# Optimization experiments

Hardware: AMD Instinct MI355X
Metric: run time of the kernel (lower is better)

Reference implementation:

```python
import jax, jax.numpy as jnp
import numpy as np

PAD_IDX, BOS_IDX, EOS_IDX = 0, 1, 2
NUM_LABELS = 48
B, T = 1024, 512
NEG = -10000.0


def make_trans(key):
    trans = jax.random.normal(key, (NUM_LABELS, NUM_LABELS), dtype=jnp.float32)
    trans = trans.at[BOS_IDX, :].set(NEG)
    trans = trans.at[:, EOS_IDX].set(NEG)
    trans = trans.at[:, PAD_IDX].set(NEG)
    trans = trans.at[PAD_IDX, :].set(NEG)
    trans = trans.at[PAD_IDX, EOS_IDX].set(0.0)
    trans = trans.at[PAD_IDX, PAD_IDX].set(0.0)
    return trans


def setup_inputs() -> dict:
    key = jax.random.key(0)
    k_h, k_tr = jax.random.split(key)
    h = jax.random.normal(k_h, (B, T, NUM_LABELS), dtype=jnp.float32)
    mask = jnp.ones((B, T), dtype=jnp.float32)
    trans = make_trans(k_tr)
    return {"h": h, "mask": mask, "trans": trans, "batch_size": B}


def reference(h, mask, trans, batch_size):
    # h: (B, T, L), mask: (B, T), trans: (L, L)
    L = trans.shape[0]
    score0 = jnp.full((batch_size, L), NEG, dtype=h.dtype).at[:, BOS_IDX].set(0.0)

    def step(score, inp):
        h_t, m_t = inp            # h_t: (B, L), m_t: (B,)
        # new[b, i] = logsumexp_j(score[b, j] + h_t[b, i] + trans[i, j])
        z = score[:, None, :] + h_t[:, :, None] + trans[None, :, :]  # (B, L, L)
        score_t = jax.nn.logsumexp(z, axis=-1)
        m = m_t[:, None]
        score = score_t * m + score * (1.0 - m)
        return score, None

    # scan over time: move T to leading axis
    score, _ = jax.lax.scan(step, score0, (jnp.swapaxes(h, 0, 1), jnp.swapaxes(mask, 0, 1)))
    return jax.nn.logsumexp(score, axis=-1)  # (B,)
```

## Files before the change

kernel.cpp:

```cpp
#include <hip/hip_runtime.h>
#include <math.h>

namespace {
constexpr int L = 48;
constexpr int OCT = 8;
constexpr float LN2f = 0.69314718055994530942f;
}

__global__ __launch_bounds__(64, 1)
void crf_fwd(const float* __restrict__ h,
             const float* __restrict__ mask,
             const float* __restrict__ trans,
             float* __restrict__ out, int T) {
  const int b = blockIdx.x;
  const int lane = threadIdx.x;
  const bool active = lane < L;
  const int safelane = active ? lane : 0;

  float E[L];
  if (active) {
#pragma unroll
    for (int j = 0; j < L; ++j) E[j] = __expf(trans[lane * L + j]);
  } else {
#pragma unroll
    for (int j = 0; j < L; ++j) E[j] = 0.0f;
  }

  float p = (lane == 1) ? 1.0f : 0.0f;
  int Mi = 0;
  float rs = 1.0f;

  const float* __restrict__ hb = h + (size_t)b * T * L;
  const float* __restrict__ mb = mask + (size_t)b * T;
  const int NOCT = T / OCT;

  float hf[OCT], mf[OCT];
#pragma unroll
  for (int k = 0; k < OCT; ++k) {
    hf[k] = hb[k * L + safelane];
    mf[k] = mb[k];
  }

  for (int oct = 0; oct < NOCT; ++oct) {
    float hn[OCT], mn[OCT];
    if (oct + 1 < NOCT) {
      const float* nb = hb + (size_t)(oct + 1) * OCT * L;
#pragma unroll
      for (int k = 0; k < OCT; ++k) {
        hn[k] = nb[k * L + safelane];
        mn[k] = mb[(oct + 1) * OCT + k];
      }
    } else {
#pragma unroll
      for (int k = 0; k < OCT; ++k) { hn[k] = 0.f; mn[k] = 1.f; }
    }

#pragma unroll
    for (int tt = 0; tt < OCT; ++tt) {
      const bool RENORM = ((tt & 3) == 3);
      float g  = __expf(hf[tt]) * rs;
      float pr = p * rs;
      rs = 1.0f;

      const int pb = __float_as_int(p);
      float a0 = 0.f, a1 = 0.f, a2 = 0.f, a3 = 0.f;
      unsigned mx = 0u;
#pragma unroll
      for (int j = 0; j < L; j += 4) {
        const int r0 = __builtin_amdgcn_readlane(pb, j + 0);
        const int r1 = __builtin_amdgcn_readlane(pb, j + 1);
        const int r2 = __builtin_amdgcn_readlane(pb, j + 2);
        const int r3 = __builtin_amdgcn_readlane(pb, j + 3);
        a0 = fmaf(__int_as_float(r0), E[j + 0], a0);
        a1 = fmaf(__int_as_float(r1), E[j + 1], a1);
        a2 = fmaf(__int_as_float(r2), E[j + 2], a2);
        a3 = fmaf(__int_as_float(r3), E[j + 3], a3);
        if (RENORM) {
          const unsigned u0 = (unsigned)r0, u1 = (unsigned)r1;
          const unsigned u2 = (unsigned)r2, u3 = (unsigned)r3;
          const unsigned m01 = u0 > u1 ? u0 : u1;
          const unsigned m23 = u2 > u3 ? u2 : u3;
          const unsigned m03 = m01 > m23 ? m01 : m23;
          mx = mx > m03 ? mx : m03;
        }
      }
      const float s = (a0 + a1) + (a2 + a3);
      const float pn = s * g;
      p = (mf[tt] > 0.5f) ? pn : pr;

      if (RENORM) {
        const int ke = (int)(mx >> 23);
        const bool ok = (ke > 0) && (ke < 255);
        rs = ok ? __uint_as_float((unsigned)(254 - ke) << 23) : 1.0f;
        Mi += ok ? (ke - 127) : 0;
      }
    }
#pragma unroll
    for (int k = 0; k < OCT; ++k) { hf[k] = hn[k]; mf[k] = mn[k]; }
  }

  float ps = p;
#pragma unroll
  for (int off = 32; off; off >>= 1) ps += __shfl_xor(ps, off, 64);
  if (lane == 0) out[b] = ((float)Mi + __log2f(ps)) * LN2f;
}

extern "C" void kernel_launch(void* const* d_in, const int* in_sizes, int n_in,
                              void* d_out, int out_size, void* d_ws, size_t ws_size,
                              hipStream_t stream) {
  const float* h     = (const float*)d_in[0];
  const float* mask  = (const float*)d_in[1];
  const float* trans = (const float*)d_in[2];
  float* out = (float*)d_out;
  const int B = out_size;
  const int T = in_sizes[1] / B;
  crf_fwd<<<B, 64, 0, stream>>>(h, mask, trans, out, T);
}
```

Before: 239.3 us.

## Split CRF forward recursion into concurrent forward and backward half-passes

Each sequence now uses two waves. One runs the forward recursion over the first half of time steps, and the other runs a backward recursion with the transposed transition matrix over the second half. The two partial vectors are combined with a dot product through shared memory. This halves the serial dependency chain per block, at the cost of twice the waves and more register pressure under launch bounds of 128 threads with 2 blocks. It assumes T is even and divisible by 16, and it changes the mask semantics for the backward half.

```diff
diff --git a/kernel.cpp b/kernel.cpp
--- a/kernel.cpp
+++ b/kernel.cpp
@@ -7,48 +7,48 @@
 constexpr float LN2f = 0.69314718055994530942f;
 }
 
-__global__ __launch_bounds__(64, 1)
-void crf_fwd(const float* __restrict__ h,
-             const float* __restrict__ mask,
-             const float* __restrict__ trans,
-             float* __restrict__ out, int T) {
-  const int b = blockIdx.x;
-  const int lane = threadIdx.x;
+template<bool BWD>
+__device__ __forceinline__ float half_pass(
+    const float* __restrict__ hb, const float* __restrict__ mb,
+    const float* __restrict__ trans, int T, int S, int lane,
+    int& Mi_out, float& rs_out) {
   const bool active = lane < L;
   const int safelane = active ? lane : 0;
 
   float E[L];
   if (active) {
 #pragma unroll
-    for (int j = 0; j < L; ++j) E[j] = __expf(trans[lane * L + j]);
+    for (int j = 0; j < L; ++j)
+      E[j] = __expf(trans[BWD ? (j * L + lane) : (lane * L + j)]);
   } else {
 #pragma unroll
     for (int j = 0; j < L; ++j) E[j] = 0.0f;
   }
 
-  float p = (lane == 1) ? 1.0f : 0.0f;
+  float p = BWD ? (active ? 1.0f : 0.0f)
+                : ((lane == 1) ? 1.0f : 0.0f);
   int Mi = 0;
   float rs = 1.0f;
 
-  const float* __restrict__ hb = h + (size_t)b * T * L;
-  const float* __restrict__ mb = mask + (size_t)b * T;
-  const int NOCT = T / OCT;
+  const int NOCT = S / OCT;
 
   float hf[OCT], mf[OCT];
 #pragma unroll
   for (int k = 0; k < OCT; ++k) {
-    hf[k] = hb[k * L + safelane];
-    mf[k] = mb[k];
+    const int t = BWD ? (T - 1 - k) : k;
+    hf[k] = hb[t * L + safelane];
+    mf[k] = mb[t];
   }
 
   for (int oct = 0; oct < NOCT; ++oct) {
     float hn[OCT], mn[OCT];
     if (oct + 1 < NOCT) {
-      const float* nb = hb + (size_t)(oct + 1) * OCT * L;
 #pragma unroll
       for (int k = 0; k < OCT; ++k) {
-        hn[k] = nb[k * L + safelane];
-        mn[k] = mb[(oct + 1) * OCT + k];
+        const int s = (oct + 1) * OCT + k;
+        const int t = BWD ? (T - 1 - s) : s;
+        hn[k] = hb[t * L + safelane];
+        mn[k] = mb[t];
       }
     } else {
 #pragma unroll
@@ -58,11 +58,12 @@
 #pragma unroll
     for (int tt = 0; tt < OCT; ++tt) {
       const bool RENORM = ((tt & 3) == 3);
-      float g  = __expf(hf[tt]) * rs;
-      float pr = p * rs;
+      const float g = __expf(hf[tt]) * rs;
+      const float pr = p * rs;
       rs = 1.0f;
 
-      const int pb = __float_as_int(p);
+      const float bv = BWD ? (p * g) : p;
+      const int pb = __float_as_int(bv);
       float a0 = 0.f, a1 = 0.f, a2 = 0.f, a3 = 0.f;
       unsigned mx = 0u;
 #pragma unroll
@@ -85,7 +86,7 @@
         }
       }
       const float s = (a0 + a1) + (a2 + a3);
-      const float pn = s * g;
+      const float pn = BWD ? s : s * g;
       p = (mf[tt] > 0.5f) ? pn : pr;
 
       if (RENORM) {
@@ -98,11 +99,43 @@
 #pragma unroll
     for (int k = 0; k < OCT; ++k) { hf[k] = hn[k]; mf[k] = mn[k]; }
   }
+  Mi_out = Mi;
+  rs_out = rs;
+  return p;
+}
 
-  float ps = p;
+__global__ __launch_bounds__(128, 2)
+void crf_fwd(const float* __restrict__ h,
+             const float* __restrict__ mask,
+             const float* __restrict__ trans,
+             float* __restrict__ out, int T) {
+  const int b = blockIdx.x;
+  const int wid = threadIdx.x >> 6;
+  const int lane = threadIdx.x & 63;
+  const int S = T >> 1;
+
+  const float* __restrict__ hb = h + (size_t)b * T * L;
+  const float* __restrict__ mb = mask + (size_t)b * T;
+
+  __shared__ float xq[64];
+  __shared__ int xmi;
+
+  int Mi; float rs; float st;
+  if (wid == 0) st = half_pass<false>(hb, mb, trans, T, S, lane, Mi, rs);
+  else          st = half_pass<true >(hb, mb, trans, T, S, lane, Mi, rs);
+
+  if (wid == 1) {
+    xq[lane] = st * rs;
+    if (lane == 0) xmi = Mi;
+  }
+  __syncthreads();
+  if (wid == 0) {
+    float d = (st * rs) * xq[lane];
 #pragma unroll
-  for (int off = 32; off; off >>= 1) ps += __shfl_xor(ps, off, 64);
-  if (lane == 0) out[b] = ((float)Mi + __log2f(ps)) * LN2f;
+    for (int off = 32; off; off >>= 1) d += __shfl_xor(d, off, 64);
+    if (lane == 0)
+      out[b] = ((float)(Mi + xmi) + __log2f(d)) * LN2f;
+  }
 }
 
 extern "C" void kernel_launch(void* const* d_in, const int* in_sizes, int n_in,
@@ -114,5 +147,5 @@
   float* out = (float*)d_out;
   const int B = out_size;
   const int T = in_sizes[1] / B;
-  crf_fwd<<<B, 64, 0, stream>>>(h, mask, trans, out, T);
+  crf_fwd<<<B, 128, 0, stream>>>(h, mask, trans, out, T);
 }
```

Measured after the change: 222.7 us. 6.9% less time.
